# Kernel tuning notes

Hardware: AMD Instinct MI355X
Metric: run time of the kernel (lower is better)

The kernel has to match this reference:

```python
import jax, jax.numpy as jnp
import numpy as np

UP = 2


def _lpf_rect(N, cutoff):
    # ideal lowpass rect over full-FFT frequency axis (with Nyquist 0.5 fix)
    cutoff_low = int((N * cutoff) // 2)
    cutoff_high = int(N - cutoff_low)
    rect = np.ones(N, dtype=np.float32)
    rect[cutoff_low + 1:cutoff_high] = 0.0
    if (N * cutoff) % 2 == 0:
        rect[cutoff_low] = 0.5
        rect[cutoff_high] = 0.5
    return rect


def _recon_rect(N, cutoff):
    # reconstruction rect for zero-insertion upsampling (no Nyquist halving)
    cutoff_low = int((N * cutoff) // 2)
    cutoff_high = int(N - cutoff_low)
    rect = np.ones(N, dtype=np.float32)
    rect[cutoff_low + 1:cutoff_high] = 0.0
    return rect


def _rfft2_mask(rect_h, rect_w):
    # outer product mask on rfft2 grid: full H axis x half W axis
    half_w = rect_w.shape[0] // 2 + 1
    return jnp.asarray(rect_h[:, None] * rect_w[None, :half_w])


def setup_inputs() -> dict:
    key = jax.random.key(0)
    x = jax.random.normal(key, (32, 128, 64, 64), dtype=jnp.float32)
    # PolyAct default init_coef (buffer, non-trainable)
    coef = jnp.array([0.0169394634313126, 0.5, 0.3078363963999393, 0.0],
                     dtype=jnp.float32)
    return {"x": x, "coef": coef}


def reference(x, coef):
    B, C, H, W = x.shape
    Hu, Wu = H * UP, W * UP

    # ---- UpsampleRFFT: zero-insertion then ideal reconstruction filter ----
    xu = jnp.zeros((B, C, Hu, Wu), x.dtype).at[:, :, ::UP, ::UP].set(x)
    recon_mask = _rfft2_mask(_recon_rect(Hu, 1.0 / UP), _recon_rect(Wu, 1.0 / UP))
    f = jnp.fft.rfft2(xu) * (UP * UP) * recon_mask
    xu = jnp.fft.irfft2(f, s=(Hu, Wu))

    # ---- PolyAct: calc_polynomial loops range(2, deg) with deg=3, so only
    # terms up to x^2 are used (coef[3] is never applied) ----
    y = coef[0] + coef[1] * xu + coef[2] * xu * xu

    # ---- LPF_RFFT with cutoff = 1/up ----
    lpf_mask = _rfft2_mask(_lpf_rect(Hu, 1.0 / UP), _lpf_rect(Wu, 1.0 / UP))
    y = jnp.fft.irfft2(jnp.fft.rfft2(y) * lpf_mask, s=(Hu, Wu))

    # ---- decimate back to original resolution ----
    return y[:, :, ::UP, ::UP]
```

## Files before the change

kernel.cpp:

```cpp
#include <hip/hip_runtime.h>
#include <math.h>


typedef short short8 __attribute__((ext_vector_type(8)));
typedef float f32x16 __attribute__((ext_vector_type(16)));

#define LSH 68

__device__ __forceinline__ short f2bf(float f) {
  unsigned u = __float_as_uint(f);
  u += 0x7FFFu + ((u >> 16) & 1u);
  return (short)(u >> 16);
}
__device__ __forceinline__ float bf2f(short s) {
  return __uint_as_float(((unsigned)(unsigned short)s) << 16);
}
__device__ __forceinline__ short8 ldrow(const short* p) {
  union { unsigned u[4]; short8 s; } v;
  const uint2 lo = *(const uint2*)p;
  const uint2 hi = *(const uint2*)(p + 4);
  v.u[0] = lo.x; v.u[1] = lo.y; v.u[2] = hi.x; v.u[3] = hi.y;
  return v.s;
}
__device__ __forceinline__ unsigned pk2(short a, short b) {
  return (unsigned)(unsigned short)a | ((unsigned)(unsigned short)b << 16);
}

__global__ void uppolyact_setup(unsigned* __restrict__ flag,
                                float* __restrict__ gws,
                                short* __restrict__ ftw) {
  if (*flag == 0xC0FFEEu) return;
  __shared__ float g64s[64];
  const int tid = threadIdx.x;
  if (tid < 64) {
    const int d = 2 * tid + 1;
    float s = 1.0f;
    for (int k = 1; k <= 32; ++k) {
      const int qq = (k * d) & 127;
      s += 2.0f * cosf((float)M_PI * (1.0f / 64.0f) * (float)qq);
    }
    const float gv = s * (1.0f / 64.0f);
    g64s[tid] = gv;
    gws[tid] = gv;
  }
  __syncthreads();
#pragma unroll
  for (int e = 0; e < 4; ++e) {
    const int entry = tid + 256 * e;
    const int s_ = entry >> 6, ln = entry & 63;
    const int t_ = s_ >> 3, blk = (s_ >> 2) & 1, kk = s_ & 3;
    const int basei = kk * 16 + (ln >> 5) * 8 - (ln & 31) - 32 * blk;
    short* dst = &ftw[(s_ * 64 + ln) * 8];
#pragma unroll
    for (int j = 0; j < 8; ++j) {
      const int i0 = basei + j;
      const int idx = t_ ? ((-i0) & 63) : (i0 & 63);
      dst[j] = f2bf(g64s[idx]);
    }
  }
  __syncthreads();
  if (tid == 0) *flag = 0xC0FFEEu;
}

template <bool PRE>
__global__ __launch_bounds__(256, 3) void uppolyact_kernel(
    const float* __restrict__ x, const float* __restrict__ coef,
    float* __restrict__ out, const float* __restrict__ gws,
    const short* __restrict__ ftw) {
  __shared__ __align__(16) short Xr[64 * LSH];
  __shared__ __align__(16) short XcZ[64 * LSH];
  __shared__ __align__(16) short LrU[64 * LSH];
  __shared__ __align__(16) short Zoo[64 * LSH];
  __shared__ __align__(16) short ftab[16 * 64 * 8];
  __shared__ float g64[64];
  __shared__ float tvec[64], uvec[64], sRv[64], Luv[64];
  __shared__ float sigv;

  const int tid = threadIdx.x;
  const int lane = tid & 63;
  const int w = tid >> 6;
  const int q = lane >> 5;
  const int l31 = lane & 31;
  const int rb = w >> 1, cb = w & 1;
  const int jcol = cb * 32 + l31;
  const size_t base = (size_t)blockIdx.x * 4096;
  const float* xb = x + base;

  float xcur[16];
#pragma unroll
  for (int r = 0; r < 16; ++r) {
    const int irow = rb * 32 + (r & 3) + 4 * q + 8 * (r >> 2);
    xcur[r] = xb[irow * 64 + jcol];
  }

  float4 t0, t1, t2, t3;
  if (PRE) {
    const float4* fsrc = (const float4*)ftw;
    t0 = fsrc[tid];
    t1 = fsrc[tid + 256];
    t2 = fsrc[tid + 512];
    t3 = fsrc[tid + 768];
    if (tid < 64) g64[tid] = gws[tid];
  } else {
    if (tid < 64) {
      const int d = 2 * tid + 1;
      float s = 1.0f;
      for (int k = 1; k <= 32; ++k) {
        const int qq = (k * d) & 127;
        s += 2.0f * cosf((float)M_PI * (1.0f / 64.0f) * (float)qq);
      }
      g64[tid] = s * (1.0f / 64.0f);
    }
  }

#pragma unroll
  for (int k = 0; k < 4; ++k) {
    const int irowb = rb * 32 + 4 * q + 8 * k;
    short b[4];
#pragma unroll
    for (int j = 0; j < 4; ++j) {
      b[j] = f2bf(xcur[4 * k + j]);
      Xr[(irowb + j) * LSH + jcol] = b[j];
    }
    uint2 p;
    p.x = pk2(b[0], b[1]);
    p.y = pk2(b[2], b[3]);
    *(uint2*)&XcZ[jcol * LSH + irowb] = p;
  }
  if (PRE) {
    float4* fdst = (float4*)ftab;
    fdst[tid] = t0;
    fdst[tid + 256] = t1;
    fdst[tid + 512] = t2;
    fdst[tid + 768] = t3;
  }
  __syncthreads();

  if (!PRE) {
#pragma unroll
    for (int e = 0; e < 4; ++e) {
      const int entry = tid + 256 * e;
      const int s_ = entry >> 6, ln = entry & 63;
      const int t_ = s_ >> 3, blk = (s_ >> 2) & 1, kk = s_ & 3;
      const int basei = kk * 16 + (ln >> 5) * 8 - (ln & 31) - 32 * blk;
      short* dst = &ftab[(s_ * 64 + ln) * 8];
#pragma unroll
      for (int j = 0; j < 8; ++j) {
        const int i0 = basei + j;
        const int idx = t_ ? ((-i0) & 63) : (i0 & 63);
        dst[j] = f2bf(g64[idx]);
      }
    }
  }
  {
    const int o = tid >> 1, h = tid & 1;
    const short* src = (o < 64) ? &XcZ[o * LSH + 32 * h]
                                : &Xr[(o - 64) * LSH + 32 * h];
    float acc = 0.0f;
#pragma unroll
    for (int p = 0; p < 4; ++p) {
      const short8 v = ldrow(src + 8 * p);
#pragma unroll
      for (int j = 0; j < 8; ++j) {
        const float f = bf2f(v[j]);
        acc += (j & 1) ? -f : f;
      }
    }
    acc += __shfl_xor(acc, 1);
    if (h == 0) {
      if (o < 64) tvec[o] = acc; else uvec[o - 64] = acc;
    }
  }
  __syncthreads();

  f32x16 Rt, Lt;
#pragma unroll
  for (int r = 0; r < 16; ++r) { Rt[r] = 0.0f; Lt[r] = 0.0f; }
#pragma unroll
  for (int kk = 0; kk < 4; ++kk) {
    const short8 aR = *(const short8*)&ftab[(((2 + rb) * 4 + kk) * 64 + lane) * 8];
    const short8 bR = ldrow(&Xr[(cb * 32 + l31) * LSH + kk * 16 + q * 8]);
    Rt = __builtin_amdgcn_mfma_f32_32x32x16_bf16(aR, bR, Rt, 0, 0, 0);
    const short8 aL = ldrow(&XcZ[(rb * 32 + l31) * LSH + kk * 16 + q * 8]);
    const short8 bL = *(const short8*)&ftab[(((2 + cb) * 4 + kk) * 64 + lane) * 8];
    Lt = __builtin_amdgcn_mfma_f32_32x32x16_bf16(aL, bL, Lt, 0, 0, 0);
  }
  {
    const int o = tid >> 1, h = tid & 1;
    const int o63 = o & 63;
    const float* vsrc = (o < 64) ? tvec : uvec;
    float acc = 0.0f;
#pragma unroll
    for (int p = 0; p < 32; ++p) {
      const int m = 32 * h + p;
      acc += vsrc[m] * g64[(o63 - m) & 63];
    }
    acc += __shfl_xor(acc, 1);
    if (h == 0) {
      if (o < 64) sRv[o] = acc; else Luv[o - 64] = acc;
    }
  }
  if (w == 0) {
    float sv = (lane & 1) ? -tvec[lane] : tvec[lane];
#pragma unroll
    for (int d_ = 1; d_ < 64; d_ <<= 1) sv += __shfl_xor(sv, d_);
    if (lane == 0) sigv = sv;
  }
  __syncthreads();

  float zoe[16];
  {
    const int icol = cb * 32 + l31;
    const float sgi = (icol & 1) ? -1.0f : 1.0f;
#pragma unroll
    for (int k = 0; k < 4; ++k) {
      const int jb = rb * 32 + 4 * q + 8 * k;
      short ze[4], zl[4];
#pragma unroll
      for (int t = 0; t < 4; ++t) {
        const int r = 4 * k + t;
        const int jrow = jb + t;
        const float sgj = (jrow & 1) ? -1.0f : 1.0f;
        const float veo = Rt[r] + sgi * sRv[jrow] * (1.0f / 64.0f);
        ze[t] = f2bf(veo * veo);
        zl[t] = f2bf(Lt[r]);
        const float voe = Lt[r] + Luv[icol] * sgj * (1.0f / 64.0f);
        zoe[r] = voe * voe;
      }
      uint2 pz, pl;
      pz.x = pk2(ze[0], ze[1]); pz.y = pk2(ze[2], ze[3]);
      pl.x = pk2(zl[0], zl[1]); pl.y = pk2(zl[2], zl[3]);
      *(uint2*)&XcZ[icol * LSH + jb] = pz;
      *(uint2*)&LrU[icol * LSH + jb] = pl;
    }
  }
  __syncthreads();

  f32x16 OOt;
#pragma unroll
  for (int r = 0; r < 16; ++r) OOt[r] = 0.0f;
#pragma unroll
  for (int kk = 0; kk < 4; ++kk) {
    const short8 a = *(const short8*)&ftab[(((2 + rb) * 4 + kk) * 64 + lane) * 8];
    const short8 b = ldrow(&LrU[(cb * 32 + l31) * LSH + kk * 16 + q * 8]);
    OOt = __builtin_amdgcn_mfma_f32_32x32x16_bf16(a, b, OOt, 0, 0, 0);
  }
  {
    const int icol = cb * 32 + l31;
#pragma unroll
    for (int k = 0; k < 4; ++k) {
      const int jb = rb * 32 + 4 * q + 8 * k;
      short zo[4];
#pragma unroll
      for (int t = 0; t < 4; ++t) {
        const int r = 4 * k + t;
        zo[t] = f2bf(OOt[r] * OOt[r]);
      }
      uint2 p;
      p.x = pk2(zo[0], zo[1]); p.y = pk2(zo[2], zo[3]);
      *(uint2*)&Zoo[icol * LSH + jb] = p;
    }
  }
  __syncthreads();

  f32x16 Ut, Wv;
#pragma unroll
  for (int r = 0; r < 16; ++r) { Ut[r] = zoe[r]; Wv[r] = 0.0f; }
#pragma unroll
  for (int kk = 0; kk < 4; ++kk) {
    const short8 aU = *(const short8*)&ftab[(((0 + rb) * 4 + kk) * 64 + lane) * 8];
    const short8 bU = ldrow(&Zoo[(cb * 32 + l31) * LSH + kk * 16 + q * 8]);
    Ut = __builtin_amdgcn_mfma_f32_32x32x16_bf16(aU, bU, Ut, 0, 0, 0);
    const short8 aW = ldrow(&XcZ[(rb * 32 + l31) * LSH + kk * 16 + q * 8]);
    const short8 bW = *(const short8*)&ftab[(((0 + cb) * 4 + kk) * 64 + lane) * 8];
    Wv = __builtin_amdgcn_mfma_f32_32x32x16_bf16(aW, bW, Wv, 0, 0, 0);
  }
#pragma unroll
  for (int r = 0; r < 16; ++r) {
    const int jrow = rb * 32 + (r & 3) + 4 * q + 8 * (r >> 2);
    const int icol = cb * 32 + l31;
    LrU[jrow * LSH + icol] = f2bf(Ut[r]);
  }
  __syncthreads();

  f32x16 Vv;
#pragma unroll
  for (int r = 0; r < 16; ++r) Vv[r] = 0.0f;
#pragma unroll
  for (int kk = 0; kk < 4; ++kk) {
    const short8 a = *(const short8*)&ftab[(((0 + rb) * 4 + kk) * 64 + lane) * 8];
    const short8 b = ldrow(&LrU[(cb * 32 + l31) * LSH + kk * 16 + q * 8]);
    Vv = __builtin_amdgcn_mfma_f32_32x32x16_bf16(a, b, Vv, 0, 0, 0);
  }

  const float c0 = coef[0], c1 = coef[1];
  const float c2q = 0.25f * coef[2];
  float* ob = out + base;
#pragma unroll
  for (int r = 0; r < 16; ++r) {
    const int irow = rb * 32 + (r & 3) + 4 * q + 8 * (r >> 2);
    const float sgi = (irow & 1) ? -1.0f : 1.0f;
    const float sgj = (jcol & 1) ? -1.0f : 1.0f;
    const float xv_ = bf2f(f2bf(xcur[r]));
    const float vee = xv_ + (sgi * tvec[jcol] + uvec[irow] * sgj) * (1.0f / 64.0f) +
                      sgi * sgj * sigv * (1.0f / 4096.0f);
    const float zee = vee * vee;
    ob[irow * 64 + jcol] = c0 + c1 * xcur[r] + c2q * (zee + Vv[r] + Wv[r]);
  }
}

extern "C" void kernel_launch(void* const* d_in, const int* in_sizes, int n_in,
                              void* d_out, int out_size, void* d_ws,
                              size_t ws_size, hipStream_t stream) {
  const float* x = (const float*)d_in[0];
  const float* coef = (const float*)d_in[1];
  float* out = (float*)d_out;
  const int channels = out_size / 4096;
  const bool pre = (d_ws != nullptr && ws_size >= 16896);
  if (pre) {
    unsigned* flag = (unsigned*)d_ws;
    float* gws = (float*)((char*)d_ws + 256);
    short* ftw = (short*)((char*)d_ws + 512);
    uppolyact_setup<<<dim3(1), dim3(256), 0, stream>>>(flag, gws, ftw);
    uppolyact_kernel<true><<<dim3(channels), dim3(256), 0, stream>>>(
        x, coef, out, gws, ftw);
  } else {
    uppolyact_kernel<false><<<dim3(channels), dim3(256), 0, stream>>>(
        x, coef, out, nullptr, nullptr);
  }
}
```

Before: 133.2 us.

## Hold filter fragments in registers from global table, drop LDS table, raise occupancy

The precomputed bf16 DFT-filter fragment table moves to a device-global array built once by a setup kernel (guarded by a flag). The shared-memory copy is removed and each wave loads its MFMA operand fragments straight into registers, reusing them across several matrix multiplies. The no-workspace fallback path is dropped. Less LDS per block and a launch bound of 4 blocks per CU aim to raise occupancy and cut LDS traffic, at the cost of more VGPR pressure and possible spills.

```diff
diff --git a/kernel.cpp b/kernel.cpp
--- a/kernel.cpp
+++ b/kernel.cpp
@@ -6,6 +6,10 @@
 typedef float f32x16 __attribute__((ext_vector_type(16)));
 
 #define LSH 68
+
+__device__ unsigned g_flag;
+__device__ float g_gws[64];
+__device__ __align__(16) short g_ftw[16 * 64 * 8];
 
 __device__ __forceinline__ short f2bf(float f) {
   unsigned u = __float_as_uint(f);
@@ -26,10 +30,8 @@
   return (unsigned)(unsigned short)a | ((unsigned)(unsigned short)b << 16);
 }
 
-__global__ void uppolyact_setup(unsigned* __restrict__ flag,
-                                float* __restrict__ gws,
-                                short* __restrict__ ftw) {
-  if (*flag == 0xC0FFEEu) return;
+__global__ void uppolyact_setup() {
+  if (g_flag == 0xC0FFEEu) return;
   __shared__ float g64s[64];
   const int tid = threadIdx.x;
   if (tid < 64) {
@@ -41,7 +43,7 @@
     }
     const float gv = s * (1.0f / 64.0f);
     g64s[tid] = gv;
-    gws[tid] = gv;
+    g_gws[tid] = gv;
   }
   __syncthreads();
 #pragma unroll
@@ -50,7 +52,7 @@
     const int s_ = entry >> 6, ln = entry & 63;
     const int t_ = s_ >> 3, blk = (s_ >> 2) & 1, kk = s_ & 3;
     const int basei = kk * 16 + (ln >> 5) * 8 - (ln & 31) - 32 * blk;
-    short* dst = &ftw[(s_ * 64 + ln) * 8];
+    short* dst = &g_ftw[(s_ * 64 + ln) * 8];
 #pragma unroll
     for (int j = 0; j < 8; ++j) {
       const int i0 = basei + j;
@@ -59,19 +61,16 @@
     }
   }
   __syncthreads();
-  if (tid == 0) *flag = 0xC0FFEEu;
-}
-
-template <bool PRE>
-__global__ __launch_bounds__(256, 3) void uppolyact_kernel(
+  if (tid == 0) g_flag = 0xC0FFEEu;
+}
+
+__global__ __launch_bounds__(256, 4) void uppolyact_kernel(
     const float* __restrict__ x, const float* __restrict__ coef,
-    float* __restrict__ out, const float* __restrict__ gws,
-    const short* __restrict__ ftw) {
+    float* __restrict__ out) {
   __shared__ __align__(16) short Xr[64 * LSH];
   __shared__ __align__(16) short XcZ[64 * LSH];
   __shared__ __align__(16) short LrU[64 * LSH];
   __shared__ __align__(16) short Zoo[64 * LSH];
-  __shared__ __align__(16) short ftab[16 * 64 * 8];
   __shared__ float g64[64];
   __shared__ float tvec[64], uvec[64], sRv[64], Luv[64];
   __shared__ float sigv;
@@ -85,6 +84,7 @@
   const int jcol = cb * 32 + l31;
   const size_t base = (size_t)blockIdx.x * 4096;
   const float* xb = x + base;
+  const short8* ft8 = (const short8*)g_ftw;
 
   float xcur[16];
 #pragma unroll
@@ -93,25 +93,13 @@
     xcur[r] = xb[irow * 64 + jcol];
   }
 
-  float4 t0, t1, t2, t3;
-  if (PRE) {
-    const float4* fsrc = (const float4*)ftw;
-    t0 = fsrc[tid];
-    t1 = fsrc[tid + 256];
-    t2 = fsrc[tid + 512];
-    t3 = fsrc[tid + 768];
-    if (tid < 64) g64[tid] = gws[tid];
-  } else {
-    if (tid < 64) {
-      const int d = 2 * tid + 1;
-      float s = 1.0f;
-      for (int k = 1; k <= 32; ++k) {
-        const int qq = (k * d) & 127;
-        s += 2.0f * cosf((float)M_PI * (1.0f / 64.0f) * (float)qq);
-      }
-      g64[tid] = s * (1.0f / 64.0f);
-    }
-  }
+  short8 fA[4], fB[4];
+#pragma unroll
+  for (int kk = 0; kk < 4; ++kk) {
+    fA[kk] = ft8[((2 + rb) * 4 + kk) * 64 + lane];
+    fB[kk] = ft8[((2 + cb) * 4 + kk) * 64 + lane];
+  }
+  if (tid < 64) g64[tid] = g_gws[tid];
 
 #pragma unroll
   for (int k = 0; k < 4; ++k) {
@@ -127,31 +115,8 @@
     p.y = pk2(b[2], b[3]);
     *(uint2*)&XcZ[jcol * LSH + irowb] = p;
   }
-  if (PRE) {
-    float4* fdst = (float4*)ftab;
-    fdst[tid] = t0;
-    fdst[tid + 256] = t1;
-    fdst[tid + 512] = t2;
-    fdst[tid + 768] = t3;
-  }
-  __syncthreads();
-
-  if (!PRE) {
-#pragma unroll
-    for (int e = 0; e < 4; ++e) {
-      const int entry = tid + 256 * e;
-      const int s_ = entry >> 6, ln = entry & 63;
-      const int t_ = s_ >> 3, blk = (s_ >> 2) & 1, kk = s_ & 3;
-      const int basei = kk * 16 + (ln >> 5) * 8 - (ln & 31) - 32 * blk;
-      short* dst = &ftab[(s_ * 64 + ln) * 8];
-#pragma unroll
-      for (int j = 0; j < 8; ++j) {
-        const int i0 = basei + j;
-        const int idx = t_ ? ((-i0) & 63) : (i0 & 63);
-        dst[j] = f2bf(g64[idx]);
-      }
-    }
-  }
+  __syncthreads();
+
   {
     const int o = tid >> 1, h = tid & 1;
     const short* src = (o < 64) ? &XcZ[o * LSH + 32 * h]
@@ -178,12 +143,10 @@
   for (int r = 0; r < 16; ++r) { Rt[r] = 0.0f; Lt[r] = 0.0f; }
 #pragma unroll
   for (int kk = 0; kk < 4; ++kk) {
-    const short8 aR = *(const short8*)&ftab[(((2 + rb) * 4 + kk) * 64 + lane) * 8];
     const short8 bR = ldrow(&Xr[(cb * 32 + l31) * LSH + kk * 16 + q * 8]);
-    Rt = __builtin_amdgcn_mfma_f32_32x32x16_bf16(aR, bR, Rt, 0, 0, 0);
+    Rt = __builtin_amdgcn_mfma_f32_32x32x16_bf16(fA[kk], bR, Rt, 0, 0, 0);
     const short8 aL = ldrow(&XcZ[(rb * 32 + l31) * LSH + kk * 16 + q * 8]);
-    const short8 bL = *(const short8*)&ftab[(((2 + cb) * 4 + kk) * 64 + lane) * 8];
-    Lt = __builtin_amdgcn_mfma_f32_32x32x16_bf16(aL, bL, Lt, 0, 0, 0);
+    Lt = __builtin_amdgcn_mfma_f32_32x32x16_bf16(aL, fB[kk], Lt, 0, 0, 0);
   }
   {
     const int o = tid >> 1, h = tid & 1;
@@ -236,14 +199,19 @@
   }
   __syncthreads();
 
+  short8 fU[4], fW[4];
+#pragma unroll
+  for (int kk = 0; kk < 4; ++kk) {
+    fU[kk] = ft8[((0 + rb) * 4 + kk) * 64 + lane];
+    fW[kk] = ft8[((0 + cb) * 4 + kk) * 64 + lane];
+  }
   f32x16 OOt;
 #pragma unroll
   for (int r = 0; r < 16; ++r) OOt[r] = 0.0f;
 #pragma unroll
   for (int kk = 0; kk < 4; ++kk) {
-    const short8 a = *(const short8*)&ftab[(((2 + rb) * 4 + kk) * 64 + lane) * 8];
     const short8 b = ldrow(&LrU[(cb * 32 + l31) * LSH + kk * 16 + q * 8]);
-    OOt = __builtin_amdgcn_mfma_f32_32x32x16_bf16(a, b, OOt, 0, 0, 0);
+    OOt = __builtin_amdgcn_mfma_f32_32x32x16_bf16(fA[kk], b, OOt, 0, 0, 0);
   }
   {
     const int icol = cb * 32 + l31;
@@ -268,12 +236,10 @@
   for (int r = 0; r < 16; ++r) { Ut[r] = zoe[r]; Wv[r] = 0.0f; }
 #pragma unroll
   for (int kk = 0; kk < 4; ++kk) {
-    const short8 aU = *(const short8*)&ftab[(((0 + rb) * 4 + kk) * 64 + lane) * 8];
     const short8 bU = ldrow(&Zoo[(cb * 32 + l31) * LSH + kk * 16 + q * 8]);
-    Ut = __builtin_amdgcn_mfma_f32_32x32x16_bf16(aU, bU, Ut, 0, 0, 0);
+    Ut = __builtin_amdgcn_mfma_f32_32x32x16_bf16(fU[kk], bU, Ut, 0, 0, 0);
     const short8 aW = ldrow(&XcZ[(rb * 32 + l31) * LSH + kk * 16 + q * 8]);
-    const short8 bW = *(const short8*)&ftab[(((0 + cb) * 4 + kk) * 64 + lane) * 8];
-    Wv = __builtin_amdgcn_mfma_f32_32x32x16_bf16(aW, bW, Wv, 0, 0, 0);
+    Wv = __builtin_amdgcn_mfma_f32_32x32x16_bf16(aW, fW[kk], Wv, 0, 0, 0);
   }
 #pragma unroll
   for (int r = 0; r < 16; ++r) {
@@ -288,9 +254,8 @@
   for (int r = 0; r < 16; ++r) Vv[r] = 0.0f;
 #pragma unroll
   for (int kk = 0; kk < 4; ++kk) {
-    const short8 a = *(const short8*)&ftab[(((0 + rb) * 4 + kk) * 64 + lane) * 8];
     const short8 b = ldrow(&LrU[(cb * 32 + l31) * LSH + kk * 16 + q * 8]);
-    Vv = __builtin_amdgcn_mfma_f32_32x32x16_bf16(a, b, Vv, 0, 0, 0);
+    Vv = __builtin_amdgcn_mfma_f32_32x32x16_bf16(fU[kk], b, Vv, 0, 0, 0);
   }
 
   const float c0 = coef[0], c1 = coef[1];
@@ -316,16 +281,6 @@
   const float* coef = (const float*)d_in[1];
   float* out = (float*)d_out;
   const int channels = out_size / 4096;
-  const bool pre = (d_ws != nullptr && ws_size >= 16896);
-  if (pre) {
-    unsigned* flag = (unsigned*)d_ws;
-    float* gws = (float*)((char*)d_ws + 256);
-    short* ftw = (short*)((char*)d_ws + 512);
-    uppolyact_setup<<<dim3(1), dim3(256), 0, stream>>>(flag, gws, ftw);
-    uppolyact_kernel<true><<<dim3(channels), dim3(256), 0, stream>>>(
-        x, coef, out, gws, ftw);
-  } else {
-    uppolyact_kernel<false><<<dim3(channels), dim3(256), 0, stream>>>(
-        x, coef, out, nullptr, nullptr);
-  }
-}
+  uppolyact_setup<<<dim3(1), dim3(256), 0, stream>>>();
+  uppolyact_kernel<<<dim3(channels), dim3(256), 0, stream>>>(x, coef, out);
+}
```

Measured after the change: 126.5 us. 1.05x faster.
